# Kernel optimization log

Measured on AMD Instinct MI355X. Metric: run time of the kernel, lower is better.

The kernel has to match this reference:

```python
import jax, jax.numpy as jnp
import numpy as np

SPARSITY_PROB = 0.1
CAUSAL = True
B, H, S, D = 2, 16, 2048, 64


def _make_mask(key, seq_len, sparsity_prob, causal):
    # random_mask = rand < p, optionally AND causal tril, then force diagonal True
    m = jax.random.uniform(key, (seq_len, seq_len)) < sparsity_prob
    if causal:
        m = m & jnp.tril(jnp.ones((seq_len, seq_len), dtype=bool))
    idx = jnp.arange(seq_len)
    m = m.at[idx, idx].set(True)
    return m


def setup_inputs() -> dict:
    key = jax.random.key(0)
    kq, kk, kv, km = jax.random.split(key, 4)
    query = jax.random.normal(kq, (B, H, S, D), dtype=jnp.float32)
    k_ = jax.random.normal(kk, (B, H, S, D), dtype=jnp.float32)
    v_ = jax.random.normal(kv, (B, H, S, D), dtype=jnp.float32)
    mask = _make_mask(km, S, SPARSITY_PROB, CAUSAL)
    return {"query": query, "key": k_, "value": v_, "mask": mask}


def reference(query, key, value, mask):
    # Masked attention: softmax over the selected positions of each row is
    # mathematically identical to the per-row gather+softmax in the original.
    # mask: [S, S] bool, shared across batch and heads; every row has at least
    # the diagonal True, so no fully-masked rows.
    head_dim = query.shape[-1]
    scale = 1.0 / jnp.sqrt(jnp.asarray(head_dim, dtype=query.dtype))
    scores = jnp.einsum("bhqd,bhkd->bhqk", query, key) * scale  # [B,H,S,S]
    scores = jnp.where(mask[None, None, :, :], scores, -jnp.inf)
    attn = jax.nn.softmax(scores, axis=-1)
    return jnp.einsum("bhqk,bhkd->bhqd", attn, value)
```

## Files before the change

kernel.cpp:

```cpp
#include <hip/hip_runtime.h>
#include <hip/hip_bf16.h>

#define SEQ 2048
#define HD 64
#define NBH 32
#define SCALE 0.125f
#define QSC 0.18033688011112042f

typedef __attribute__((ext_vector_type(4)))  float    f32x4;
typedef __attribute__((ext_vector_type(16))) float    f32x16;
typedef __attribute__((ext_vector_type(8)))  short    bf16x8;
typedef __attribute__((ext_vector_type(4)))  unsigned u32x4;

__device__ inline short f2bf(float f) {
    unsigned u = __builtin_bit_cast(unsigned, f);
    unsigned r = u + 0x7FFFu + ((u >> 16) & 1u);
    return (short)(r >> 16);
}

__device__ inline unsigned cvt2(float lo, float hi) {
    unsigned d;
    asm("v_cvt_pk_bf16_f32 %0, %1, %2" : "=v"(d) : "v"(lo), "v"(hi));
    return d;
}

__global__ void detect_mask_kernel(const unsigned char* __restrict__ m, int n, int* flag) {
    if (threadIdx.x == 0) *flag = (m[n - 1] != 0) ? 1 : 4;
}

__global__ __launch_bounds__(256)
void prep_kernel(const unsigned char* __restrict__ m, const int* __restrict__ flag,
                 const float* __restrict__ K, const float* __restrict__ V,
                 unsigned* __restrict__ bits, short* __restrict__ Kb,
                 short* __restrict__ Vt) {
    __shared__ short t[64][65];
    const int b = blockIdx.x, tid = threadIdx.x;
    if (b < 512) {
        const int idx = b * 256 + tid;
        const int row = idx >> 6, w = idx & 63;
        const size_t base = (size_t)row * SEQ + w * 32;
        unsigned word = 0;
        if (*flag == 1) {
            #pragma unroll
            for (int i = 0; i < 32; ++i) word |= (unsigned)(m[base + i] != 0) << i;
        } else {
            const unsigned* m32 = (const unsigned*)m;
            #pragma unroll
            for (int i = 0; i < 32; ++i) word |= (unsigned)(m32[base + i] != 0) << i;
        }
        bits[(size_t)w * SEQ + row] = word;
    } else if (b < 2560) {
        const int g = (b - 512) * 256 + tid;
        const size_t i = (size_t)g * 8;
        f32x4 a = *(const f32x4*)(K + i);
        f32x4 c = *(const f32x4*)(K + i + 4);
        bf16x8 o;
        #pragma unroll
        for (int j = 0; j < 4; ++j) { o[j] = f2bf(a[j]); o[4 + j] = f2bf(c[j]); }
        const int row = g >> 3;
        const int c8  = g & 7;
        const int bh  = row >> 11;
        const int r   = row & 2047;
        const int tt  = r >> 5;
        const int la  = r & 31;
        *(bf16x8*)(Kb + ((size_t)bh * 64 + tt) * 2048 + (c8 * 32 + la) * 8) = o;
    } else {
        const int bb = b - 2560;
        const int s0 = (bb & 31) * 64, bh = bb >> 5;
        const float* Vb = V + (size_t)bh * SEQ * HD;
        const int sr = tid >> 6, d = tid & 63;
        #pragma unroll
        for (int i = 0; i < 16; ++i) {
            const int s = i * 4 + sr;
            t[s][d] = f2bf(Vb[(size_t)(s0 + s) * HD + d]);
        }
        __syncthreads();
        short* o = Vt + (size_t)bh * HD * SEQ;
        const int dr = tid >> 6, sl = tid & 63;
        #pragma unroll
        for (int i = 0; i < 16; ++i) {
            const int dd = i * 4 + dr;
            const int s = s0 + sl;
            const int k = s & 31;
            const int p = (k & ~12) | ((k & 8) >> 1) | ((k & 4) << 1);
            const int mm = ((dd >> 5) << 1) | (p >> 4);
            const int hh = (p >> 3) & 1;
            o[(size_t)(s >> 5) * 2048 + ((mm * 2 + hh) * 32 + (dd & 31)) * 8 + (p & 7)] = t[sl][dd];
        }
    }
}

__global__ __launch_bounds__(256, 2)
void attn_shared_kernel(const float* __restrict__ Q, const short* __restrict__ Kb,
                        const short* __restrict__ Vt, const unsigned* __restrict__ bitsT,
                        float* __restrict__ Out) {
    __shared__ __align__(16) short kbuf[2][2048];
    __shared__ __align__(16) short vbuf[2][2048];
    __shared__ short oacc[4][32][72];

    const int id   = blockIdx.x;
    const int bh   = id & 31;
    const int qg   = 15 - (id >> 5);
    const int tid  = threadIdx.x;
    const int wid  = tid >> 6;
    const int lane = tid & 63;
    const int la   = lane & 31;
    const int h    = lane >> 5;
    const int q0w  = qg * 128 + wid * 32;
    const int nt   = qg * 4 + 4;
    const size_t base = (size_t)bh * SEQ * HD;

    bf16x8 qf[4];
    {
        const float* qp = Q + base + (size_t)(q0w + la) * HD + h * 8;
        #pragma unroll
        for (int j = 0; j < 4; ++j) {
            f32x4 a0 = *(const f32x4*)(qp + j * 16);
            f32x4 a1 = *(const f32x4*)(qp + j * 16 + 4);
            #pragma unroll
            for (int i = 0; i < 4; ++i) {
                qf[j][i]     = f2bf(a0[i] * QSC);
                qf[j][4 + i] = f2bf(a1[i] * QSC);
            }
        }
    }

    f32x16 acc_o0 = {0,0,0,0,0,0,0,0,0,0,0,0,0,0,0,0};
    f32x16 acc_o1 = {0,0,0,0,0,0,0,0,0,0,0,0,0,0,0,0};
    float l_run = 0.f;

    const short* Ktg = Kb + (size_t)bh * 64 * 2048;
    const short* Vtg = Vt + (size_t)bh * 64 * 2048;
    const unsigned* bq = bitsT + q0w + la;
    const int bp = 4 * h;

    {
        bf16x8 sk = *(const bf16x8*)(Ktg + (size_t)tid * 8);
        bf16x8 sv = *(const bf16x8*)(Vtg + (size_t)tid * 8);
        *(bf16x8*)(&kbuf[0][0] + tid * 8) = sk;
        *(bf16x8*)(&vbuf[0][0] + tid * 8) = sv;
    }
    unsigned mw = bq[0];

    int cur = 0;
    for (int t = 0; t < nt; ++t) {
        __syncthreads();

        const short* kb = &kbuf[cur][0];
        const short* vb = &vbuf[cur][0];
        bf16x8 kfa = *(const bf16x8*)(kb + lane * 8);
        bf16x8 kfb = *(const bf16x8*)(kb + 512 + lane * 8);
        bf16x8 kfc = *(const bf16x8*)(kb + 1024 + lane * 8);
        bf16x8 kfd = *(const bf16x8*)(kb + 1536 + lane * 8);
        bf16x8 vf00 = *(const bf16x8*)(vb + lane * 8);
        bf16x8 vf01 = *(const bf16x8*)(vb + 512 + lane * 8);
        bf16x8 vf10 = *(const bf16x8*)(vb + 1024 + lane * 8);
        bf16x8 vf11 = *(const bf16x8*)(vb + 1536 + lane * 8);

        const int tn = (t + 1 < nt) ? t + 1 : t;
        bf16x8 sk = *(const bf16x8*)(Ktg + (size_t)tn * 2048 + tid * 8);
        bf16x8 sv = *(const bf16x8*)(Vtg + (size_t)tn * 2048 + tid * 8);
        unsigned nmw = bq[(size_t)tn * SEQ];

        f32x16 sA = {0,0,0,0,0,0,0,0,0,0,0,0,0,0,0,0};
        f32x16 sB = {0,0,0,0,0,0,0,0,0,0,0,0,0,0,0,0};
        __builtin_amdgcn_s_setprio(1);
        sA = __builtin_amdgcn_mfma_f32_32x32x16_bf16(kfa, qf[0], sA, 0, 0, 0);
        sB = __builtin_amdgcn_mfma_f32_32x32x16_bf16(kfc, qf[2], sB, 0, 0, 0);
        sA = __builtin_amdgcn_mfma_f32_32x32x16_bf16(kfb, qf[1], sA, 0, 0, 0);
        sB = __builtin_amdgcn_mfma_f32_32x32x16_bf16(kfd, qf[3], sB, 0, 0, 0);
        __builtin_amdgcn_s_setprio(0);
        f32x16 s = sA + sB;

        #pragma unroll
        for (int r = 0; r < 16; ++r) {
            float e = __builtin_amdgcn_exp2f(s[r]);
            s[r] = ((mw >> (bp + (r & 3) + 8 * (r >> 2))) & 1u) ? e : 0.f;
        }
        float ps = ((s[0] + s[1]) + (s[2] + s[3])) + ((s[4] + s[5]) + (s[6] + s[7]));
        ps += ((s[8] + s[9]) + (s[10] + s[11])) + ((s[12] + s[13]) + (s[14] + s[15]));
        l_run += ps;

        u32x4 t1 = {cvt2(s[0], s[1]),  cvt2(s[2], s[3]),
                    cvt2(s[4], s[5]),  cvt2(s[6], s[7])};
        u32x4 t2 = {cvt2(s[8], s[9]),  cvt2(s[10], s[11]),
                    cvt2(s[12], s[13]), cvt2(s[14], s[15])};
        bf16x8 pb1 = __builtin_bit_cast(bf16x8, t1);
        bf16x8 pb2 = __builtin_bit_cast(bf16x8, t2);

        __builtin_amdgcn_s_setprio(1);
        acc_o0 = __builtin_amdgcn_mfma_f32_32x32x16_bf16(vf00, pb1, acc_o0, 0, 0, 0);
        acc_o1 = __builtin_amdgcn_mfma_f32_32x32x16_bf16(vf10, pb1, acc_o1, 0, 0, 0);
        acc_o0 = __builtin_amdgcn_mfma_f32_32x32x16_bf16(vf01, pb2, acc_o0, 0, 0, 0);
        acc_o1 = __builtin_amdgcn_mfma_f32_32x32x16_bf16(vf11, pb2, acc_o1, 0, 0, 0);
        __builtin_amdgcn_s_setprio(0);

        *(bf16x8*)(&kbuf[cur ^ 1][0] + tid * 8) = sk;
        *(bf16x8*)(&vbuf[cur ^ 1][0] + tid * 8) = sv;

        mw = nmw;
        cur ^= 1;
    }

    {
        const float l_full = l_run + __shfl_xor(l_run, 32);
        const float invw = 1.f / l_full;
        unsigned short* orow = (unsigned short*)&oacc[wid][la][0];
        #pragma unroll
        for (int g = 0; g < 4; ++g) {
            const int d0 = 8 * g + 4 * h;
            unsigned w0 = cvt2(acc_o0[4 * g + 0] * invw, acc_o0[4 * g + 1] * invw);
            unsigned w1 = cvt2(acc_o0[4 * g + 2] * invw, acc_o0[4 * g + 3] * invw);
            unsigned w2 = cvt2(acc_o1[4 * g + 0] * invw, acc_o1[4 * g + 1] * invw);
            unsigned w3 = cvt2(acc_o1[4 * g + 2] * invw, acc_o1[4 * g + 3] * invw);
            *(unsigned*)&orow[d0]      = w0;
            *(unsigned*)&orow[d0 + 2]  = w1;
            *(unsigned*)&orow[d0 + 32] = w2;
            *(unsigned*)&orow[d0 + 34] = w3;
        }
    }
    __syncthreads();

    {
        const int q  = tid >> 3;
        const int dc = (tid & 7) * 8;
        #pragma unroll
        for (int k = 0; k < 4; ++k) {
            u32x4 pk = *(const u32x4*)&oacc[k][q][dc];
            float o[8];
            #pragma unroll
            for (int j = 0; j < 4; ++j) {
                o[2 * j]     = __builtin_bit_cast(float, (pk[j] & 0xFFFFu) << 16);
                o[2 * j + 1] = __builtin_bit_cast(float, pk[j] & 0xFFFF0000u);
            }
            float* op = Out + base + (size_t)(qg * 128 + k * 32 + q) * HD + dc;
            f32x4 o0v = {o[0], o[1], o[2], o[3]};
            f32x4 o1v = {o[4], o[5], o[6], o[7]};
            *(f32x4*)op       = o0v;
            *(f32x4*)(op + 4) = o1v;
        }
    }
}

__global__ __launch_bounds__(256)
void attn_kernel(const float* __restrict__ Q, const float* __restrict__ K,
                 const float* __restrict__ V, const unsigned char* __restrict__ mask,
                 const int* __restrict__ flag, float* __restrict__ Out) {
    __shared__ short plds[4][16][40];
    const int esz  = *flag;
    const int bh   = blockIdx.y;
    const int wid  = threadIdx.x >> 6;
    const int lane = threadIdx.x & 63;
    const int l16  = lane & 15;
    const int hi   = lane >> 4;
    const int q0   = blockIdx.x * 64 + wid * 16;
    const size_t base = (size_t)bh * SEQ * HD;
    const float* Qb = Q + base;
    const float* Kb = K + base;
    const float* Vb = V + base;
    const unsigned int* mask32 = (const unsigned int*)mask;
    bf16x8 qf[2];
    {
        const float* qp = Qb + (size_t)(q0 + l16) * HD + hi * 8;
        f32x4 a0 = *(const f32x4*)(qp);
        f32x4 a1 = *(const f32x4*)(qp + 4);
        f32x4 a2 = *(const f32x4*)(qp + 32);
        f32x4 a3 = *(const f32x4*)(qp + 36);
        #pragma unroll
        for (int i = 0; i < 4; ++i) {
            qf[0][i] = f2bf(a0[i]); qf[0][4 + i] = f2bf(a1[i]);
            qf[1][i] = f2bf(a2[i]); qf[1][4 + i] = f2bf(a3[i]);
        }
    }
    f32x4 acc_o[4] = {f32x4{0,0,0,0}, f32x4{0,0,0,0}, f32x4{0,0,0,0}, f32x4{0,0,0,0}};
    float m_run[4], l_run[4];
    #pragma unroll
    for (int j = 0; j < 4; ++j) { m_run[j] = -__builtin_inff(); l_run[j] = 0.f; }
    const int kv_end = q0 + 16;
    for (int kv = 0; kv < kv_end; kv += 32) {
        f32x4 acc_s[2] = {f32x4{0,0,0,0}, f32x4{0,0,0,0}};
        #pragma unroll
        for (int t = 0; t < 2; ++t) {
            const float* kp = Kb + (size_t)(kv + 16 * t + l16) * HD + hi * 8;
            f32x4 b0 = *(const f32x4*)(kp);
            f32x4 b1 = *(const f32x4*)(kp + 4);
            f32x4 b2 = *(const f32x4*)(kp + 32);
            f32x4 b3 = *(const f32x4*)(kp + 36);
            bf16x8 kf0, kf1;
            #pragma unroll
            for (int i = 0; i < 4; ++i) {
                kf0[i] = f2bf(b0[i]); kf0[4 + i] = f2bf(b1[i]);
                kf1[i] = f2bf(b2[i]); kf1[4 + i] = f2bf(b3[i]);
            }
            acc_s[t] = __builtin_amdgcn_mfma_f32_16x16x32_bf16(qf[0], kf0, acc_s[t], 0, 0, 0);
            acc_s[t] = __builtin_amdgcn_mfma_f32_16x16x32_bf16(qf[1], kf1, acc_s[t], 0, 0, 0);
        }
        float s[2][4];
        #pragma unroll
        for (int t = 0; t < 2; ++t) {
            const int k = kv + 16 * t + l16;
            #pragma unroll
            for (int j = 0; j < 4; ++j) {
                const int qrow = q0 + hi * 4 + j;
                const size_t midx = (size_t)qrow * SEQ + k;
                const bool mv = (esz == 1) ? (mask[midx] != 0) : (mask32[midx] != 0);
                s[t][j] = mv ? acc_s[t][j] * SCALE : -__builtin_inff();
            }
        }
        float mnew[4], r[4];
        #pragma unroll
        for (int j = 0; j < 4; ++j) {
            float v = fmaxf(s[0][j], s[1][j]);
            #pragma unroll
            for (int off = 1; off < 16; off <<= 1) v = fmaxf(v, __shfl_xor(v, off));
            mnew[j] = fmaxf(m_run[j], v);
            r[j] = (m_run[j] > -__builtin_inff()) ? __expf(m_run[j] - mnew[j]) : 0.f;
        }
        float p[2][4];
        #pragma unroll
        for (int j = 0; j < 4; ++j) {
            float ps = 0.f;
            #pragma unroll
            for (int t = 0; t < 2; ++t) {
                p[t][j] = (s[t][j] > -__builtin_inff()) ? __expf(s[t][j] - mnew[j]) : 0.f;
                ps += p[t][j];
            }
            #pragma unroll
            for (int off = 1; off < 16; off <<= 1) ps += __shfl_xor(ps, off);
            l_run[j] = l_run[j] * r[j] + ps;
            m_run[j] = mnew[j];
            #pragma unroll
            for (int t2 = 0; t2 < 4; ++t2) acc_o[t2][j] *= r[j];
        }
        #pragma unroll
        for (int t = 0; t < 2; ++t)
            #pragma unroll
            for (int j = 0; j < 4; ++j)
                plds[wid][hi * 4 + j][16 * t + l16] = f2bf(p[t][j]);
        bf16x8 pa = *(bf16x8*)&plds[wid][l16][hi * 8];
        #pragma unroll
        for (int t2 = 0; t2 < 4; ++t2) {
            const float* vp = Vb + (size_t)(kv + hi * 8) * HD + 16 * t2 + l16;
            bf16x8 vf;
            #pragma unroll
            for (int i = 0; i < 8; ++i) vf[i] = f2bf(vp[(size_t)i * HD]);
            acc_o[t2] = __builtin_amdgcn_mfma_f32_16x16x32_bf16(pa, vf, acc_o[t2], 0, 0, 0);
        }
    }
    #pragma unroll
    for (int j = 0; j < 4; ++j) {
        const float inv = 1.f / l_run[j];
        const int qrow = q0 + hi * 4 + j;
        float* op = Out + base + (size_t)qrow * HD + l16;
        #pragma unroll
        for (int t2 = 0; t2 < 4; ++t2) op[16 * t2] = acc_o[t2][j] * inv;
    }
}

extern "C" void kernel_launch(void* const* d_in, const int* in_sizes, int n_in,
                              void* d_out, int out_size, void* d_ws, size_t ws_size,
                              hipStream_t stream) {
    const float* Q = (const float*)d_in[0];
    const float* K = (const float*)d_in[1];
    const float* V = (const float*)d_in[2];
    const unsigned char* mask = (const unsigned char*)d_in[3];

    const size_t bitsB = (size_t)SEQ * (SEQ / 32) * 4;
    const size_t kvB   = (size_t)NBH * SEQ * HD * 2;
    const size_t need  = bitsB + 2 * kvB + 256;

    if (ws_size >= need) {
        unsigned* bits = (unsigned*)d_ws;
        short* Kb = (short*)((char*)d_ws + bitsB);
        short* Vt = (short*)((char*)d_ws + bitsB + kvB);
        int* flag = (int*)((char*)d_ws + bitsB + 2 * kvB);

        detect_mask_kernel<<<dim3(1), dim3(64), 0, stream>>>(mask, in_sizes[3], flag);
        prep_kernel<<<dim3(3584), dim3(256), 0, stream>>>(mask, flag, K, V, bits, Kb, Vt);
        attn_shared_kernel<<<dim3(512), dim3(256), 0, stream>>>(Q, Kb, Vt, bits, (float*)d_out);
    } else {
        int* flag = (int*)d_ws;
        detect_mask_kernel<<<dim3(1), dim3(64), 0, stream>>>(mask, in_sizes[3], flag);
        attn_kernel<<<dim3(SEQ / 64, NBH), dim3(256), 0, stream>>>(Q, K, V, mask, flag, (float*)d_out);
    }
}
```

Baseline: 62.39 us.

## Process two K/V tiles per barrier and interleave block scheduling order

The main loop now stages two 32-key K/V tiles per iteration in a doubled shared-memory buffer, so each __syncthreads covers two tiles of MFMA work and the global loads for the next pair are issued together. This halves barrier count and deepens prefetch, at the cost of twice the LDS footprint and more live registers, which may reduce occupancy. The query-group mapping also changes so that blocks with id >= 256 go in ascending order instead of descending, which alters the causal load-balance ordering. The loop assumes nt is even, which holds since nt = 4*qg+4.

```diff
diff --git a/kernel.cpp b/kernel.cpp
--- a/kernel.cpp
+++ b/kernel.cpp
@@ -94,13 +94,13 @@
 void attn_shared_kernel(const float* __restrict__ Q, const short* __restrict__ Kb,
                         const short* __restrict__ Vt, const unsigned* __restrict__ bitsT,
                         float* __restrict__ Out) {
-    __shared__ __align__(16) short kbuf[2][2048];
-    __shared__ __align__(16) short vbuf[2][2048];
+    __shared__ __align__(16) short kbuf[2][2][2048];
+    __shared__ __align__(16) short vbuf[2][2][2048];
     __shared__ short oacc[4][32][72];
 
     const int id   = blockIdx.x;
     const int bh   = id & 31;
-    const int qg   = 15 - (id >> 5);
+    const int qg   = (id < 256) ? (15 - (id >> 5)) : ((id - 256) >> 5);
     const int tid  = threadIdx.x;
     const int wid  = tid >> 6;
     const int lane = tid & 63;
@@ -134,20 +134,7 @@
     const unsigned* bq = bitsT + q0w + la;
     const int bp = 4 * h;
 
-    {
-        bf16x8 sk = *(const bf16x8*)(Ktg + (size_t)tid * 8);
-        bf16x8 sv = *(const bf16x8*)(Vtg + (size_t)tid * 8);
-        *(bf16x8*)(&kbuf[0][0] + tid * 8) = sk;
-        *(bf16x8*)(&vbuf[0][0] + tid * 8) = sv;
-    }
-    unsigned mw = bq[0];
-
-    int cur = 0;
-    for (int t = 0; t < nt; ++t) {
-        __syncthreads();
-
-        const short* kb = &kbuf[cur][0];
-        const short* vb = &vbuf[cur][0];
+    auto body = [&](const short* kb, const short* vb, unsigned mwx) {
         bf16x8 kfa = *(const bf16x8*)(kb + lane * 8);
         bf16x8 kfb = *(const bf16x8*)(kb + 512 + lane * 8);
         bf16x8 kfc = *(const bf16x8*)(kb + 1024 + lane * 8);
@@ -156,11 +143,6 @@
         bf16x8 vf01 = *(const bf16x8*)(vb + 512 + lane * 8);
         bf16x8 vf10 = *(const bf16x8*)(vb + 1024 + lane * 8);
         bf16x8 vf11 = *(const bf16x8*)(vb + 1536 + lane * 8);
-
-        const int tn = (t + 1 < nt) ? t + 1 : t;
-        bf16x8 sk = *(const bf16x8*)(Ktg + (size_t)tn * 2048 + tid * 8);
-        bf16x8 sv = *(const bf16x8*)(Vtg + (size_t)tn * 2048 + tid * 8);
-        unsigned nmw = bq[(size_t)tn * SEQ];
 
         f32x16 sA = {0,0,0,0,0,0,0,0,0,0,0,0,0,0,0,0};
         f32x16 sB = {0,0,0,0,0,0,0,0,0,0,0,0,0,0,0,0};
@@ -175,7 +157,7 @@
         #pragma unroll
         for (int r = 0; r < 16; ++r) {
             float e = __builtin_amdgcn_exp2f(s[r]);
-            s[r] = ((mw >> (bp + (r & 3) + 8 * (r >> 2))) & 1u) ? e : 0.f;
+            s[r] = ((mwx >> (bp + (r & 3) + 8 * (r >> 2))) & 1u) ? e : 0.f;
         }
         float ps = ((s[0] + s[1]) + (s[2] + s[3])) + ((s[4] + s[5]) + (s[6] + s[7]));
         ps += ((s[8] + s[9]) + (s[10] + s[11])) + ((s[12] + s[13]) + (s[14] + s[15]));
@@ -194,11 +176,43 @@
         acc_o0 = __builtin_amdgcn_mfma_f32_32x32x16_bf16(vf01, pb2, acc_o0, 0, 0, 0);
         acc_o1 = __builtin_amdgcn_mfma_f32_32x32x16_bf16(vf11, pb2, acc_o1, 0, 0, 0);
         __builtin_amdgcn_s_setprio(0);
-
-        *(bf16x8*)(&kbuf[cur ^ 1][0] + tid * 8) = sk;
-        *(bf16x8*)(&vbuf[cur ^ 1][0] + tid * 8) = sv;
-
-        mw = nmw;
+    };
+
+    {
+        bf16x8 k0 = *(const bf16x8*)(Ktg + (size_t)tid * 8);
+        bf16x8 k1 = *(const bf16x8*)(Ktg + 2048 + (size_t)tid * 8);
+        bf16x8 v0 = *(const bf16x8*)(Vtg + (size_t)tid * 8);
+        bf16x8 v1 = *(const bf16x8*)(Vtg + 2048 + (size_t)tid * 8);
+        *(bf16x8*)(&kbuf[0][0][0] + tid * 8) = k0;
+        *(bf16x8*)(&kbuf[0][1][0] + tid * 8) = k1;
+        *(bf16x8*)(&vbuf[0][0][0] + tid * 8) = v0;
+        *(bf16x8*)(&vbuf[0][1][0] + tid * 8) = v1;
+    }
+    unsigned mw0 = bq[0];
+    unsigned mw1 = bq[SEQ];
+
+    int cur = 0;
+    for (int t = 0; t < nt; t += 2) {
+        __syncthreads();
+
+        const int tn0 = (t + 2 < nt) ? t + 2 : t;
+        const int tn1 = (t + 3 < nt) ? t + 3 : t;
+        bf16x8 sk0 = *(const bf16x8*)(Ktg + (size_t)tn0 * 2048 + tid * 8);
+        bf16x8 sk1 = *(const bf16x8*)(Ktg + (size_t)tn1 * 2048 + tid * 8);
+        bf16x8 sv0 = *(const bf16x8*)(Vtg + (size_t)tn0 * 2048 + tid * 8);
+        bf16x8 sv1 = *(const bf16x8*)(Vtg + (size_t)tn1 * 2048 + tid * 8);
+        unsigned nmw0 = bq[(size_t)tn0 * SEQ];
+        unsigned nmw1 = bq[(size_t)tn1 * SEQ];
+
+        body(&kbuf[cur][0][0], &vbuf[cur][0][0], mw0);
+        body(&kbuf[cur][1][0], &vbuf[cur][1][0], mw1);
+
+        *(bf16x8*)(&kbuf[cur ^ 1][0][0] + tid * 8) = sk0;
+        *(bf16x8*)(&kbuf[cur ^ 1][1][0] + tid * 8) = sk1;
+        *(bf16x8*)(&vbuf[cur ^ 1][0][0] + tid * 8) = sv0;
+        *(bf16x8*)(&vbuf[cur ^ 1][1][0] + tid * 8) = sv1;
+
+        mw0 = nmw0; mw1 = nmw1;
         cur ^= 1;
     }
 
```

Result: faster. 58.43 us (-6.4%).

## Split KV range across two blocks per query tile and reduce partial outputs

Applied to the files above, without the earlier changes.

Each 128-query tile's key/value range is split into two halves handled by separate blocks (1024 blocks instead of 512). Per-half normalized outputs and row sums go to a workspace and are combined by a new reduce kernel. K/V staging now uses global_load_lds direct-to-LDS copies, double-buffered two tiles at a time. The mask-format detect kernel is folded into prep_kernel. This targets the causal load imbalance and the launch overhead of the extra kernel. In exchange it adds a third kernel launch, extra workspace traffic, and a second bf16 rounding of partial outputs.

```diff
diff --git a/kernel.cpp b/kernel.cpp
--- a/kernel.cpp
+++ b/kernel.cpp
@@ -24,23 +24,30 @@
     return d;
 }
 
+__device__ inline void gll16(const short* g, short* l) {
+    __builtin_amdgcn_global_load_lds(
+        (__attribute__((address_space(1))) void*)(g),
+        (__attribute__((address_space(3))) void*)(l), 16, 0, 0);
+}
+
 __global__ void detect_mask_kernel(const unsigned char* __restrict__ m, int n, int* flag) {
     if (threadIdx.x == 0) *flag = (m[n - 1] != 0) ? 1 : 4;
 }
 
 __global__ __launch_bounds__(256)
-void prep_kernel(const unsigned char* __restrict__ m, const int* __restrict__ flag,
+void prep_kernel(const unsigned char* __restrict__ m, int mn,
                  const float* __restrict__ K, const float* __restrict__ V,
                  unsigned* __restrict__ bits, short* __restrict__ Kb,
                  short* __restrict__ Vt) {
     __shared__ short t[64][65];
     const int b = blockIdx.x, tid = threadIdx.x;
     if (b < 512) {
+        const bool e1 = (m[mn - 1] != 0);
         const int idx = b * 256 + tid;
         const int row = idx >> 6, w = idx & 63;
         const size_t base = (size_t)row * SEQ + w * 32;
         unsigned word = 0;
-        if (*flag == 1) {
+        if (e1) {
             #pragma unroll
             for (int i = 0; i < 32; ++i) word |= (unsigned)(m[base + i] != 0) << i;
         } else {
@@ -91,28 +98,36 @@
 }
 
 __global__ __launch_bounds__(256, 2)
-void attn_shared_kernel(const float* __restrict__ Q, const short* __restrict__ Kb,
-                        const short* __restrict__ Vt, const unsigned* __restrict__ bitsT,
-                        float* __restrict__ Out) {
-    __shared__ __align__(16) short kbuf[2][2048];
-    __shared__ __align__(16) short vbuf[2][2048];
-    __shared__ short oacc[4][32][72];
+void attn_half_kernel(const float* __restrict__ Q, const short* __restrict__ Kb,
+                      const short* __restrict__ Vt, const unsigned* __restrict__ bitsT,
+                      short* __restrict__ Oh_ws, float* __restrict__ l_ws) {
+    __shared__ __align__(16) short pool[16384];
+    short* kpool = pool;
+    short* vpool = pool + 8192;
 
     const int id   = blockIdx.x;
     const int bh   = id & 31;
-    const int qg   = 15 - (id >> 5);
+    const int s8   = (id >> 5) & 7;
+    const int g    = id >> 8;
+    int qg, half;
+    if (g == 0)      { qg = 15 - s8; half = 0; }
+    else if (g == 1) { qg = 8 + s8;  half = 1; }
+    else if (g == 2) { qg = 7 - s8;  half = 0; }
+    else             { qg = s8;      half = 1; }
+
     const int tid  = threadIdx.x;
     const int wid  = tid >> 6;
     const int lane = tid & 63;
     const int la   = lane & 31;
     const int h    = lane >> 5;
     const int q0w  = qg * 128 + wid * 32;
-    const int nt   = qg * 4 + 4;
-    const size_t base = (size_t)bh * SEQ * HD;
+    const int htiles = 2 * qg + 2;
+    const int tstart = half * htiles;
+    const int tend   = tstart + htiles;
 
     bf16x8 qf[4];
     {
-        const float* qp = Q + base + (size_t)(q0w + la) * HD + h * 8;
+        const float* qp = Q + (size_t)bh * SEQ * HD + (size_t)(q0w + la) * HD + h * 8;
         #pragma unroll
         for (int j = 0; j < 4; ++j) {
             f32x4 a0 = *(const f32x4*)(qp + j * 16);
@@ -133,21 +148,10 @@
     const short* Vtg = Vt + (size_t)bh * 64 * 2048;
     const unsigned* bq = bitsT + q0w + la;
     const int bp = 4 * h;
-
-    {
-        bf16x8 sk = *(const bf16x8*)(Ktg + (size_t)tid * 8);
-        bf16x8 sv = *(const bf16x8*)(Vtg + (size_t)tid * 8);
-        *(bf16x8*)(&kbuf[0][0] + tid * 8) = sk;
-        *(bf16x8*)(&vbuf[0][0] + tid * 8) = sv;
-    }
-    unsigned mw = bq[0];
-
-    int cur = 0;
-    for (int t = 0; t < nt; ++t) {
-        __syncthreads();
-
-        const short* kb = &kbuf[cur][0];
-        const short* vb = &vbuf[cur][0];
+    const int wl8 = wid * 512 + lane * 8;
+    const int wb  = wid * 512;
+
+    auto body = [&](const short* kb, const short* vb, unsigned mwx) {
         bf16x8 kfa = *(const bf16x8*)(kb + lane * 8);
         bf16x8 kfb = *(const bf16x8*)(kb + 512 + lane * 8);
         bf16x8 kfc = *(const bf16x8*)(kb + 1024 + lane * 8);
@@ -156,11 +160,6 @@
         bf16x8 vf01 = *(const bf16x8*)(vb + 512 + lane * 8);
         bf16x8 vf10 = *(const bf16x8*)(vb + 1024 + lane * 8);
         bf16x8 vf11 = *(const bf16x8*)(vb + 1536 + lane * 8);
-
-        const int tn = (t + 1 < nt) ? t + 1 : t;
-        bf16x8 sk = *(const bf16x8*)(Ktg + (size_t)tn * 2048 + tid * 8);
-        bf16x8 sv = *(const bf16x8*)(Vtg + (size_t)tn * 2048 + tid * 8);
-        unsigned nmw = bq[(size_t)tn * SEQ];
 
         f32x16 sA = {0,0,0,0,0,0,0,0,0,0,0,0,0,0,0,0};
         f32x16 sB = {0,0,0,0,0,0,0,0,0,0,0,0,0,0,0,0};
@@ -175,7 +174,7 @@
         #pragma unroll
         for (int r = 0; r < 16; ++r) {
             float e = __builtin_amdgcn_exp2f(s[r]);
-            s[r] = ((mw >> (bp + (r & 3) + 8 * (r >> 2))) & 1u) ? e : 0.f;
+            s[r] = ((mwx >> (bp + (r & 3) + 8 * (r >> 2))) & 1u) ? e : 0.f;
         }
         float ps = ((s[0] + s[1]) + (s[2] + s[3])) + ((s[4] + s[5]) + (s[6] + s[7]));
         ps += ((s[8] + s[9]) + (s[10] + s[11])) + ((s[12] + s[13]) + (s[14] + s[15]));
@@ -194,25 +193,54 @@
         acc_o0 = __builtin_amdgcn_mfma_f32_32x32x16_bf16(vf01, pb2, acc_o0, 0, 0, 0);
         acc_o1 = __builtin_amdgcn_mfma_f32_32x32x16_bf16(vf11, pb2, acc_o1, 0, 0, 0);
         __builtin_amdgcn_s_setprio(0);
-
-        *(bf16x8*)(&kbuf[cur ^ 1][0] + tid * 8) = sk;
-        *(bf16x8*)(&vbuf[cur ^ 1][0] + tid * 8) = sv;
-
-        mw = nmw;
+    };
+
+    gll16(Ktg + (size_t)tstart * 2048 + wl8,       kpool + wb);
+    gll16(Ktg + (size_t)(tstart + 1) * 2048 + wl8, kpool + 2048 + wb);
+    gll16(Vtg + (size_t)tstart * 2048 + wl8,       vpool + wb);
+    gll16(Vtg + (size_t)(tstart + 1) * 2048 + wl8, vpool + 2048 + wb);
+    unsigned mw0 = bq[(size_t)tstart * SEQ];
+    unsigned mw1 = bq[(size_t)(tstart + 1) * SEQ];
+
+    int cur = 0;
+    for (int t = tstart; t < tend; t += 2) {
+        __syncthreads();
+
+        if (t + 2 < tend) {
+            const int nb = (cur ^ 1) * 4096;
+            gll16(Ktg + (size_t)(t + 2) * 2048 + wl8, kpool + nb + wb);
+            gll16(Ktg + (size_t)(t + 3) * 2048 + wl8, kpool + nb + 2048 + wb);
+            gll16(Vtg + (size_t)(t + 2) * 2048 + wl8, vpool + nb + wb);
+            gll16(Vtg + (size_t)(t + 3) * 2048 + wl8, vpool + nb + 2048 + wb);
+        }
+        unsigned nmw0 = (t + 2 < tend) ? bq[(size_t)(t + 2) * SEQ] : 0u;
+        unsigned nmw1 = (t + 3 < tend) ? bq[(size_t)(t + 3) * SEQ] : 0u;
+
+        body(kpool + cur * 4096, vpool + cur * 4096, mw0);
+        body(kpool + cur * 4096 + 2048, vpool + cur * 4096 + 2048, mw1);
+
+        mw0 = nmw0; mw1 = nmw1;
         cur ^= 1;
     }
 
+    const int slot = (qg * 32 + bh) * 2 + half;
+
+    const float l_full = l_run + __shfl_xor(l_run, 32);
+    const float invw = (l_full > 0.f) ? (1.f / l_full) : 0.f;
+    if (h == 0) l_ws[(size_t)slot * 128 + wid * 32 + la] = l_full;
+
+    __syncthreads();
+
+    short (*oacc)[32][72] = (short (*)[32][72])pool;
     {
-        const float l_full = l_run + __shfl_xor(l_run, 32);
-        const float invw = 1.f / l_full;
         unsigned short* orow = (unsigned short*)&oacc[wid][la][0];
         #pragma unroll
-        for (int g = 0; g < 4; ++g) {
-            const int d0 = 8 * g + 4 * h;
-            unsigned w0 = cvt2(acc_o0[4 * g + 0] * invw, acc_o0[4 * g + 1] * invw);
-            unsigned w1 = cvt2(acc_o0[4 * g + 2] * invw, acc_o0[4 * g + 3] * invw);
-            unsigned w2 = cvt2(acc_o1[4 * g + 0] * invw, acc_o1[4 * g + 1] * invw);
-            unsigned w3 = cvt2(acc_o1[4 * g + 2] * invw, acc_o1[4 * g + 3] * invw);
+        for (int g2 = 0; g2 < 4; ++g2) {
+            const int d0 = 8 * g2 + 4 * h;
+            unsigned w0 = cvt2(acc_o0[4 * g2 + 0] * invw, acc_o0[4 * g2 + 1] * invw);
+            unsigned w1 = cvt2(acc_o0[4 * g2 + 2] * invw, acc_o0[4 * g2 + 3] * invw);
+            unsigned w2 = cvt2(acc_o1[4 * g2 + 0] * invw, acc_o1[4 * g2 + 1] * invw);
+            unsigned w3 = cvt2(acc_o1[4 * g2 + 2] * invw, acc_o1[4 * g2 + 3] * invw);
             *(unsigned*)&orow[d0]      = w0;
             *(unsigned*)&orow[d0 + 2]  = w1;
             *(unsigned*)&orow[d0 + 32] = w2;
@@ -224,22 +252,47 @@
     {
         const int q  = tid >> 3;
         const int dc = (tid & 7) * 8;
+        unsigned short* ob = (unsigned short*)Oh_ws + (size_t)slot * 8192;
         #pragma unroll
         for (int k = 0; k < 4; ++k) {
             u32x4 pk = *(const u32x4*)&oacc[k][q][dc];
-            float o[8];
-            #pragma unroll
-            for (int j = 0; j < 4; ++j) {
-                o[2 * j]     = __builtin_bit_cast(float, (pk[j] & 0xFFFFu) << 16);
-                o[2 * j + 1] = __builtin_bit_cast(float, pk[j] & 0xFFFF0000u);
-            }
-            float* op = Out + base + (size_t)(qg * 128 + k * 32 + q) * HD + dc;
-            f32x4 o0v = {o[0], o[1], o[2], o[3]};
-            f32x4 o1v = {o[4], o[5], o[6], o[7]};
-            *(f32x4*)op       = o0v;
-            *(f32x4*)(op + 4) = o1v;
-        }
-    }
+            *(u32x4*)(ob + (k * 32 + q) * 64 + dc) = pk;
+        }
+    }
+}
+
+__global__ __launch_bounds__(256)
+void reduce_kernel(const short* __restrict__ Oh_ws, const float* __restrict__ l_ws,
+                   float* __restrict__ Out) {
+    const int id = blockIdx.x;
+    const int group = id >> 2;
+    const int sub = id & 3;
+    const int qg = group >> 5, bh = group & 31;
+    const int tid = threadIdx.x;
+    const int q  = sub * 32 + (tid >> 3);
+    const int dc = (tid & 7) * 8;
+    const size_t s0 = (size_t)(group * 2);
+
+    const float l0 = l_ws[s0 * 128 + q];
+    const float l1 = l_ws[(s0 + 1) * 128 + q];
+    const float inv = 1.f / (l0 + l1);
+    u32x4 p0 = *(const u32x4*)((const unsigned short*)Oh_ws + s0 * 8192 + q * 64 + dc);
+    u32x4 p1 = *(const u32x4*)((const unsigned short*)Oh_ws + (s0 + 1) * 8192 + q * 64 + dc);
+    float o[8];
+    #pragma unroll
+    for (int j = 0; j < 4; ++j) {
+        float a0 = __builtin_bit_cast(float, (p0[j] & 0xFFFFu) << 16);
+        float a1 = __builtin_bit_cast(float, p0[j] & 0xFFFF0000u);
+        float b0 = __builtin_bit_cast(float, (p1[j] & 0xFFFFu) << 16);
+        float b1 = __builtin_bit_cast(float, p1[j] & 0xFFFF0000u);
+        o[2 * j]     = (l0 * a0 + l1 * b0) * inv;
+        o[2 * j + 1] = (l0 * a1 + l1 * b1) * inv;
+    }
+    float* op = Out + (size_t)bh * SEQ * HD + (size_t)(qg * 128 + q) * HD + dc;
+    f32x4 o0v = {o[0], o[1], o[2], o[3]};
+    f32x4 o1v = {o[4], o[5], o[6], o[7]};
+    *(f32x4*)op       = o0v;
+    *(f32x4*)(op + 4) = o1v;
 }
 
 __global__ __launch_bounds__(256)
@@ -367,17 +420,21 @@
 
     const size_t bitsB = (size_t)SEQ * (SEQ / 32) * 4;
     const size_t kvB   = (size_t)NBH * SEQ * HD * 2;
-    const size_t need  = bitsB + 2 * kvB + 256;
-
-    if (ws_size >= need) {
+    const size_t flagB = 256;
+    const size_t ohB   = (size_t)1024 * 8192 * 2;
+    const size_t lB    = (size_t)1024 * 128 * 4;
+    const size_t need_split = bitsB + 2 * kvB + flagB + ohB + lB;
+
+    if (ws_size >= need_split) {
         unsigned* bits = (unsigned*)d_ws;
         short* Kb = (short*)((char*)d_ws + bitsB);
         short* Vt = (short*)((char*)d_ws + bitsB + kvB);
-        int* flag = (int*)((char*)d_ws + bitsB + 2 * kvB);
-
-        detect_mask_kernel<<<dim3(1), dim3(64), 0, stream>>>(mask, in_sizes[3], flag);
-        prep_kernel<<<dim3(3584), dim3(256), 0, stream>>>(mask, flag, K, V, bits, Kb, Vt);
-        attn_shared_kernel<<<dim3(512), dim3(256), 0, stream>>>(Q, Kb, Vt, bits, (float*)d_out);
+        short* Oh_ws = (short*)((char*)d_ws + bitsB + 2 * kvB + flagB);
+        float* l_ws  = (float*)((char*)d_ws + bitsB + 2 * kvB + flagB + ohB);
+
+        prep_kernel<<<dim3(3584), dim3(256), 0, stream>>>(mask, in_sizes[3], K, V, bits, Kb, Vt);
+        attn_half_kernel<<<dim3(1024), dim3(256), 0, stream>>>(Q, Kb, Vt, bits, Oh_ws, l_ws);
+        reduce_kernel<<<dim3(2048), dim3(256), 0, stream>>>(Oh_ws, l_ws, (float*)d_out);
     } else {
         int* flag = (int*)d_ws;
         detect_mask_kernel<<<dim3(1), dim3(64), 0, stream>>>(mask, in_sizes[3], flag);
```

New measurement: 62.02 us. Within noise of the previous version (-0.6%).

## Stage four KV tiles per barrier, drop detect kernel, reorder block scheduling

Applied to the files above, without the earlier changes.

The attention loop now loads four 32-key K/V tiles per stage into a 64KB shared pool and double-buffers at that granularity, so it hits a barrier once per four tiles instead of every tile. The mask-format detection moves inline into the prep kernel, which removes one kernel launch. Block-to-query-group mapping changes so the second half of the blocks runs groups in ascending order, pairing long and short causal rows. The larger shared footprint (64KB per block) may lower occupancy, and it raises register pressure from the eight in-flight prefetch vectors.

```diff
diff --git a/kernel.cpp b/kernel.cpp
--- a/kernel.cpp
+++ b/kernel.cpp
@@ -29,18 +29,19 @@
 }
 
 __global__ __launch_bounds__(256)
-void prep_kernel(const unsigned char* __restrict__ m, const int* __restrict__ flag,
+void prep_kernel(const unsigned char* __restrict__ m, int mn,
                  const float* __restrict__ K, const float* __restrict__ V,
                  unsigned* __restrict__ bits, short* __restrict__ Kb,
                  short* __restrict__ Vt) {
     __shared__ short t[64][65];
     const int b = blockIdx.x, tid = threadIdx.x;
     if (b < 512) {
+        const bool e1 = (m[mn - 1] != 0);
         const int idx = b * 256 + tid;
         const int row = idx >> 6, w = idx & 63;
         const size_t base = (size_t)row * SEQ + w * 32;
         unsigned word = 0;
-        if (*flag == 1) {
+        if (e1) {
             #pragma unroll
             for (int i = 0; i < 32; ++i) word |= (unsigned)(m[base + i] != 0) << i;
         } else {
@@ -91,16 +92,16 @@
 }
 
 __global__ __launch_bounds__(256, 2)
-void attn_shared_kernel(const float* __restrict__ Q, const short* __restrict__ Kb,
-                        const short* __restrict__ Vt, const unsigned* __restrict__ bitsT,
-                        float* __restrict__ Out) {
-    __shared__ __align__(16) short kbuf[2][2048];
-    __shared__ __align__(16) short vbuf[2][2048];
-    __shared__ short oacc[4][32][72];
+void attn_shared4_kernel(const float* __restrict__ Q, const short* __restrict__ Kb,
+                         const short* __restrict__ Vt, const unsigned* __restrict__ bitsT,
+                         float* __restrict__ Out) {
+    __shared__ __align__(16) short pool[32768];
+    short* kpool = pool;
+    short* vpool = pool + 16384;
 
     const int id   = blockIdx.x;
     const int bh   = id & 31;
-    const int qg   = 15 - (id >> 5);
+    const int qg   = (id < 256) ? (15 - (id >> 5)) : ((id - 256) >> 5);
     const int tid  = threadIdx.x;
     const int wid  = tid >> 6;
     const int lane = tid & 63;
@@ -134,20 +135,7 @@
     const unsigned* bq = bitsT + q0w + la;
     const int bp = 4 * h;
 
-    {
-        bf16x8 sk = *(const bf16x8*)(Ktg + (size_t)tid * 8);
-        bf16x8 sv = *(const bf16x8*)(Vtg + (size_t)tid * 8);
-        *(bf16x8*)(&kbuf[0][0] + tid * 8) = sk;
-        *(bf16x8*)(&vbuf[0][0] + tid * 8) = sv;
-    }
-    unsigned mw = bq[0];
-
-    int cur = 0;
-    for (int t = 0; t < nt; ++t) {
-        __syncthreads();
-
-        const short* kb = &kbuf[cur][0];
-        const short* vb = &vbuf[cur][0];
+    auto body = [&](const short* kb, const short* vb, unsigned mwx) {
         bf16x8 kfa = *(const bf16x8*)(kb + lane * 8);
         bf16x8 kfb = *(const bf16x8*)(kb + 512 + lane * 8);
         bf16x8 kfc = *(const bf16x8*)(kb + 1024 + lane * 8);
@@ -156,11 +144,6 @@
         bf16x8 vf01 = *(const bf16x8*)(vb + 512 + lane * 8);
         bf16x8 vf10 = *(const bf16x8*)(vb + 1024 + lane * 8);
         bf16x8 vf11 = *(const bf16x8*)(vb + 1536 + lane * 8);
-
-        const int tn = (t + 1 < nt) ? t + 1 : t;
-        bf16x8 sk = *(const bf16x8*)(Ktg + (size_t)tn * 2048 + tid * 8);
-        bf16x8 sv = *(const bf16x8*)(Vtg + (size_t)tn * 2048 + tid * 8);
-        unsigned nmw = bq[(size_t)tn * SEQ];
 
         f32x16 sA = {0,0,0,0,0,0,0,0,0,0,0,0,0,0,0,0};
         f32x16 sB = {0,0,0,0,0,0,0,0,0,0,0,0,0,0,0,0};
@@ -175,7 +158,7 @@
         #pragma unroll
         for (int r = 0; r < 16; ++r) {
             float e = __builtin_amdgcn_exp2f(s[r]);
-            s[r] = ((mw >> (bp + (r & 3) + 8 * (r >> 2))) & 1u) ? e : 0.f;
+            s[r] = ((mwx >> (bp + (r & 3) + 8 * (r >> 2))) & 1u) ? e : 0.f;
         }
         float ps = ((s[0] + s[1]) + (s[2] + s[3])) + ((s[4] + s[5]) + (s[6] + s[7]));
         ps += ((s[8] + s[9]) + (s[10] + s[11])) + ((s[12] + s[13]) + (s[14] + s[15]));
@@ -194,17 +177,64 @@
         acc_o0 = __builtin_amdgcn_mfma_f32_32x32x16_bf16(vf01, pb2, acc_o0, 0, 0, 0);
         acc_o1 = __builtin_amdgcn_mfma_f32_32x32x16_bf16(vf11, pb2, acc_o1, 0, 0, 0);
         __builtin_amdgcn_s_setprio(0);
-
-        *(bf16x8*)(&kbuf[cur ^ 1][0] + tid * 8) = sk;
-        *(bf16x8*)(&vbuf[cur ^ 1][0] + tid * 8) = sv;
-
-        mw = nmw;
+    };
+
+    #pragma unroll
+    for (int i = 0; i < 4; ++i) {
+        bf16x8 k = *(const bf16x8*)(Ktg + (size_t)i * 2048 + tid * 8);
+        bf16x8 v = *(const bf16x8*)(Vtg + (size_t)i * 2048 + tid * 8);
+        *(bf16x8*)(kpool + i * 2048 + tid * 8) = k;
+        *(bf16x8*)(vpool + i * 2048 + tid * 8) = v;
+    }
+    unsigned mw0 = bq[0 * SEQ], mw1 = bq[1 * SEQ], mw2 = bq[2 * SEQ], mw3 = bq[3 * SEQ];
+
+    int cur = 0;
+    for (int t = 0; t < nt; t += 4) {
+        __syncthreads();
+
+        const int tb = (t + 4 < nt) ? t + 4 : t;
+        bf16x8 sk0 = *(const bf16x8*)(Ktg + (size_t)(tb + 0) * 2048 + tid * 8);
+        bf16x8 sk1 = *(const bf16x8*)(Ktg + (size_t)(tb + 1) * 2048 + tid * 8);
+        bf16x8 sk2 = *(const bf16x8*)(Ktg + (size_t)(tb + 2) * 2048 + tid * 8);
+        bf16x8 sk3 = *(const bf16x8*)(Ktg + (size_t)(tb + 3) * 2048 + tid * 8);
+        bf16x8 sv0 = *(const bf16x8*)(Vtg + (size_t)(tb + 0) * 2048 + tid * 8);
+        bf16x8 sv1 = *(const bf16x8*)(Vtg + (size_t)(tb + 1) * 2048 + tid * 8);
+        bf16x8 sv2 = *(const bf16x8*)(Vtg + (size_t)(tb + 2) * 2048 + tid * 8);
+        bf16x8 sv3 = *(const bf16x8*)(Vtg + (size_t)(tb + 3) * 2048 + tid * 8);
+        unsigned nmw0 = bq[(size_t)(tb + 0) * SEQ];
+        unsigned nmw1 = bq[(size_t)(tb + 1) * SEQ];
+        unsigned nmw2 = bq[(size_t)(tb + 2) * SEQ];
+        unsigned nmw3 = bq[(size_t)(tb + 3) * SEQ];
+
+        const short* kc = kpool + cur * 8192;
+        const short* vc = vpool + cur * 8192;
+        body(kc,        vc,        mw0);
+        body(kc + 2048, vc + 2048, mw1);
+        body(kc + 4096, vc + 4096, mw2);
+        body(kc + 6144, vc + 6144, mw3);
+
+        short* kn = kpool + (cur ^ 1) * 8192;
+        short* vn = vpool + (cur ^ 1) * 8192;
+        *(bf16x8*)(kn + tid * 8)        = sk0;
+        *(bf16x8*)(kn + 2048 + tid * 8) = sk1;
+        *(bf16x8*)(kn + 4096 + tid * 8) = sk2;
+        *(bf16x8*)(kn + 6144 + tid * 8) = sk3;
+        *(bf16x8*)(vn + tid * 8)        = sv0;
+        *(bf16x8*)(vn + 2048 + tid * 8) = sv1;
+        *(bf16x8*)(vn + 4096 + tid * 8) = sv2;
+        *(bf16x8*)(vn + 6144 + tid * 8) = sv3;
+
+        mw0 = nmw0; mw1 = nmw1; mw2 = nmw2; mw3 = nmw3;
         cur ^= 1;
     }
 
+    const float l_full = l_run + __shfl_xor(l_run, 32);
+    const float invw = 1.f / l_full;
+
+    __syncthreads();
+
+    short (*oacc)[32][72] = (short (*)[32][72])pool;
     {
-        const float l_full = l_run + __shfl_xor(l_run, 32);
-        const float invw = 1.f / l_full;
         unsigned short* orow = (unsigned short*)&oacc[wid][la][0];
         #pragma unroll
         for (int g = 0; g < 4; ++g) {
@@ -373,11 +403,9 @@
         unsigned* bits = (unsigned*)d_ws;
         short* Kb = (short*)((char*)d_ws + bitsB);
         short* Vt = (short*)((char*)d_ws + bitsB + kvB);
-        int* flag = (int*)((char*)d_ws + bitsB + 2 * kvB);
-
-        detect_mask_kernel<<<dim3(1), dim3(64), 0, stream>>>(mask, in_sizes[3], flag);
-        prep_kernel<<<dim3(3584), dim3(256), 0, stream>>>(mask, flag, K, V, bits, Kb, Vt);
-        attn_shared_kernel<<<dim3(512), dim3(256), 0, stream>>>(Q, Kb, Vt, bits, (float*)d_out);
+
+        prep_kernel<<<dim3(3584), dim3(256), 0, stream>>>(mask, in_sizes[3], K, V, bits, Kb, Vt);
+        attn_shared4_kernel<<<dim3(512), dim3(256), 0, stream>>>(Q, Kb, Vt, bits, (float*)d_out);
     } else {
         int* flag = (int*)d_ws;
         detect_mask_kernel<<<dim3(1), dim3(64), 0, stream>>>(mask, in_sizes[3], flag);
```

Measured after the change: 54.38 us. 12.8% less time.
